# Kernel tuning notes

Measured on AMD Instinct MI355X. Metric: run time of the kernel, lower is better.

## Reference

```python
import jax, jax.numpy as jnp
import numpy as np

N = 50000      # nodes (single node type 'mapping_var')
IN = 128       # in_feats
HID = 128      # hid_feats
OUT = 64       # out_feats
R = 3          # number of relations
E = 800000     # edges per relation (avg degree 16)
NEG_SLOPE = 0.01  # F.leaky_relu default


def setup_inputs() -> dict:
    key = jax.random.key(0)
    ks = jax.random.split(key, 9)
    s = 0.05
    return {
        "x": jax.random.normal(ks[0], (N, IN), jnp.float32),
        "edge_src": jax.random.randint(ks[1], (R, E), 0, N, jnp.int32),
        "edge_dst": jax.random.randint(ks[2], (R, E), 0, N, jnp.int32),
        "W0": jax.random.normal(ks[3], (R, IN, HID), jnp.float32) * s,
        "b0": jnp.zeros((R, HID), jnp.float32),
        "Wl": jax.random.normal(ks[4], (4, R, HID, HID), jnp.float32) * s,
        "bl": jnp.zeros((4, R, HID), jnp.float32),
        "Wout": jax.random.normal(ks[5], (HID, OUT), jnp.float32) * s,
        "bout": jnp.zeros((OUT,), jnp.float32),
    }


def _hetero_conv(h, edge_src, edge_dst, W, b):
    """One HeteroGraphConv layer: per-relation GraphConv (norm='both') then
    mean-aggregate across relations.  h: [N, Din], W: [R, Din, Dout]."""
    ones = jnp.ones((E,), h.dtype)
    outs = []
    for r in range(R):
        src, dst = edge_src[r], edge_dst[r]
        out_deg = jax.ops.segment_sum(ones, src, num_segments=N)
        in_deg = jax.ops.segment_sum(ones, dst, num_segments=N)
        # src-side normalization D_out^{-1/2}
        hn = h * jax.lax.rsqrt(jnp.maximum(out_deg, 1.0))[:, None]
        # gather messages along edges, sum into destinations
        agg = jax.ops.segment_sum(hn[src], dst, num_segments=N)
        # dst-side normalization D_in^{-1/2}
        agg = agg * jax.lax.rsqrt(jnp.maximum(in_deg, 1.0))[:, None]
        outs.append(agg @ W[r] + b[r])
    return jnp.mean(jnp.stack(outs, axis=0), axis=0)  # 'mean' cross-relation aggregate


def reference(x, edge_src, edge_dst, W0, b0, Wl, bl, Wout, bout):
    # Layer 0: in_feats -> hid_feats
    h = _hetero_conv(x, edge_src, edge_dst, W0, b0)
    h = jax.nn.leaky_relu(h, NEG_SLOPE)  # dropout omitted (eval mode)
    # Layers 1..4: hid -> hid; activation after all but the last
    for l in range(4):
        h = _hetero_conv(h, edge_src, edge_dst, Wl[l], bl[l])
        if l != 3:
            h = jax.nn.leaky_relu(h, NEG_SLOPE)
    # final Linear on h['mapping_var']
    return h @ Wout + bout
```

## Files before the change

### kernel.cpp

```cpp
#include <hip/hip_runtime.h>
#include <hip/hip_bf16.h>
#include <cstddef>
#include <cstdint>

#define NNODES 50000
#define NR 3
#define NE 800000
#define HIDF 128
#define OUTF 64
#define NEG_SLOPE 0.01f
#define SCAN_T 1024
#define NCHUNK ((NNODES + SCAN_T - 1) / SCAN_T)
#define KTOT (NR * HIDF)
#define KU (KTOT / 2)
#define RN (NR * NNODES)
#define CHN 4096
#define NCH ((NNODES + CHN - 1) / CHN)
#define NSEG 8
#define SEGE (NE / NSEG)

__device__ __forceinline__ float bf_lo(uint v) { return __uint_as_float(v << 16); }
__device__ __forceinline__ float bf_hi(uint v) { return __uint_as_float(v & 0xffff0000u); }
__device__ __forceinline__ uint bf_rne(float f) {
    uint u = __float_as_uint(f);
    return (u + 0x7fffu + ((u >> 16) & 1u)) >> 16;
}
__device__ __forceinline__ uint bf_pack(float a, float b) {
    return bf_rne(a) | (bf_rne(b) << 16);
}

typedef short bf16x8 __attribute__((ext_vector_type(8)));
typedef float f32x4 __attribute__((ext_vector_type(4)));
__device__ __forceinline__ bf16x8 as_bf(uint4 v) { return __builtin_bit_cast(bf16x8, v); }

__global__ __launch_bounds__(256) void k_cast_x(const float* __restrict__ x,
                                                uint* __restrict__ xb) {
    int i = blockIdx.x * blockDim.x + threadIdx.x;
    if (i >= NNODES * (HIDF / 2)) return;
    float2 v = *(const float2*)(x + (size_t)i * 2);
    xb[i] = bf_pack(v.x, v.y);
}

__global__ __launch_bounds__(256) void k_cast_w(const float* __restrict__ W0,
                                                const float* __restrict__ Wl,
                                                uint* __restrict__ wbT) {
    int idx = blockIdx.x * blockDim.x + threadIdx.x;
    if (idx >= 5 * HIDF * KU) return;
    int l = idx / (HIDF * KU);
    int rem = idx - l * (HIDF * KU);
    int t = rem / HIDF;
    int n = rem - t * HIDF;
    int r = t / 64;
    int kk = (t - r * 64) * 2;
    const float* Wsrc = (l == 0) ? W0 : Wl + (size_t)(l - 1) * NR * HIDF * HIDF;
    const float* wp = Wsrc + ((size_t)r * HIDF + kk) * HIDF + n;
    float a = wp[0];
    float b = wp[HIDF];
    wbT[(size_t)l * HIDF * KU + (size_t)n * KU + t] = bf_pack(a, b);
}

__global__ __launch_bounds__(1024) void k_seg_count(const int* __restrict__ esrc,
                                                    const int* __restrict__ edst,
                                                    int* __restrict__ sc_out,
                                                    int* __restrict__ sc_in) {
    __shared__ int cnt[CHN];
    int bid = blockIdx.x;
    int role = bid / (NR * NCH * NSEG);
    int rem = bid - role * (NR * NCH * NSEG);
    int r = rem / (NCH * NSEG);
    int rem2 = rem - r * (NCH * NSEG);
    int c = rem2 / NSEG;
    int seg = rem2 - c * NSEG;
    int lo = c * CHN;
    int hi = lo + CHN; if (hi > NNODES) hi = NNODES;
    int span = hi - lo;
    const int* arr = (role ? esrc : edst) + (size_t)r * NE + (size_t)seg * SEGE;

    for (int i = threadIdx.x; i < CHN; i += 1024) cnt[i] = 0;
    __syncthreads();

    int base = threadIdx.x * 4;
    for (int it = 0; it < SEGE; it += 4096) {
        int idx = it + base;
        if (idx < SEGE) {
            int4 v = *(const int4*)(arr + idx);
            if ((unsigned)(v.x - lo) < (unsigned)span) atomicAdd(&cnt[v.x - lo], 1);
            if ((unsigned)(v.y - lo) < (unsigned)span) atomicAdd(&cnt[v.y - lo], 1);
            if ((unsigned)(v.z - lo) < (unsigned)span) atomicAdd(&cnt[v.z - lo], 1);
            if ((unsigned)(v.w - lo) < (unsigned)span) atomicAdd(&cnt[v.w - lo], 1);
        }
    }
    __syncthreads();

    int* dst = (role ? sc_out : sc_in) + (size_t)seg * RN + r * NNODES;
    for (int i = threadIdx.x; i < span; i += 1024) dst[lo + i] = cnt[i];
}

__global__ __launch_bounds__(256) void k_merge(const int* __restrict__ sc_out,
                                               const int* __restrict__ sc_in,
                                               int* __restrict__ deg_in,
                                               int* __restrict__ xsoff,
                                               float* __restrict__ out_norm,
                                               float* __restrict__ in_norm) {
    int idx = blockIdx.x * blockDim.x + threadIdx.x;
    if (idx >= RN) return;
    int so = 0;
#pragma unroll
    for (int s = 0; s < NSEG; ++s) so += sc_out[(size_t)s * RN + idx];
    int si = 0;
#pragma unroll
    for (int s = 0; s < NSEG; ++s) {
        xsoff[(size_t)s * RN + idx] = si;
        si += sc_in[(size_t)s * RN + idx];
    }
    deg_in[idx] = si;
    out_norm[idx] = rsqrtf((float)(so > 1 ? so : 1));
    in_norm[idx]  = rsqrtf((float)(si > 1 ? si : 1));
}

__global__ __launch_bounds__(SCAN_T) void k_scan1(const int* __restrict__ deg_in,
                                                  int* __restrict__ row_ptr,
                                                  int* __restrict__ csums) {
    __shared__ int buf[SCAN_T];
    int r = blockIdx.x / NCHUNK;
    int c = blockIdx.x % NCHUNK;
    int tid = threadIdx.x;
    int i = c * SCAN_T + tid;
    int v = (i < NNODES) ? deg_in[r * NNODES + i] : 0;
    buf[tid] = v;
    __syncthreads();
    for (int off = 1; off < SCAN_T; off <<= 1) {
        int t = (tid >= off) ? buf[tid - off] : 0;
        __syncthreads();
        buf[tid] += t;
        __syncthreads();
    }
    if (i < NNODES) row_ptr[r * (NNODES + 1) + i + 1] = buf[tid];
    if (tid == SCAN_T - 1) csums[r * NCHUNK + c] = buf[SCAN_T - 1];
}

__global__ void k_scan2(const int* __restrict__ csums, int* __restrict__ coffs) {
    int r = threadIdx.x;
    if (r >= NR) return;
    int run = 0;
    for (int c = 0; c < NCHUNK; ++c) {
        coffs[r * NCHUNK + c] = run;
        run += csums[r * NCHUNK + c];
    }
}

__global__ __launch_bounds__(SCAN_T) void k_scan3(int* __restrict__ row_ptr,
                                                  const int* __restrict__ coffs) {
    int r = blockIdx.x / NCHUNK;
    int c = blockIdx.x % NCHUNK;
    int tid = threadIdx.x;
    int i = c * SCAN_T + tid;
    int off = coffs[r * NCHUNK + c];
    if (i < NNODES) row_ptr[r * (NNODES + 1) + i + 1] += off;
    if (tid == 0 && c == 0) row_ptr[r * (NNODES + 1)] = 0;
}

__global__ __launch_bounds__(1024) void k_seg_fill(const int* __restrict__ esrc,
                                                   const int* __restrict__ edst,
                                                   const int* __restrict__ row_ptr,
                                                   const int* __restrict__ xsoff,
                                                   const float* __restrict__ out_norm,
                                                   int2* __restrict__ csr_sw) {
    __shared__ int cur[CHN];
    int bid = blockIdx.x;
    int r = bid / (NCH * NSEG);
    int rem = bid - r * (NCH * NSEG);
    int c = rem / NSEG;
    int seg = rem - c * NSEG;
    int lo = c * CHN;
    int hi = lo + CHN; if (hi > NNODES) hi = NNODES;
    int span = hi - lo;
    const int* sarr = esrc + (size_t)r * NE + (size_t)seg * SEGE;
    const int* darr = edst + (size_t)r * NE + (size_t)seg * SEGE;
    const int* rp = row_ptr + r * (NNODES + 1);
    const int* xs = xsoff + (size_t)seg * RN + r * NNODES;
    const float* on = out_norm + r * NNODES;
    int2* cs = csr_sw + (size_t)r * NE;

    for (int i = threadIdx.x; i < CHN; i += 1024) cur[i] = 0;
    __syncthreads();

    int base = threadIdx.x * 4;
    for (int it = 0; it < SEGE; it += 4096) {
        int idx = it + base;
        if (idx < SEGE) {
            int4 d = *(const int4*)(darr + idx);
            int4 s = *(const int4*)(sarr + idx);
            if ((unsigned)(d.x - lo) < (unsigned)span) {
                int p = atomicAdd(&cur[d.x - lo], 1);
                cs[rp[d.x] + xs[d.x] + p] = make_int2(s.x, __float_as_int(on[s.x]));
            }
            if ((unsigned)(d.y - lo) < (unsigned)span) {
                int p = atomicAdd(&cur[d.y - lo], 1);
                cs[rp[d.y] + xs[d.y] + p] = make_int2(s.y, __float_as_int(on[s.y]));
            }
            if ((unsigned)(d.z - lo) < (unsigned)span) {
                int p = atomicAdd(&cur[d.z - lo], 1);
                cs[rp[d.z] + xs[d.z] + p] = make_int2(s.z, __float_as_int(on[s.z]));
            }
            if ((unsigned)(d.w - lo) < (unsigned)span) {
                int p = atomicAdd(&cur[d.w - lo], 1);
                cs[rp[d.w] + xs[d.w] + p] = make_int2(s.w, __float_as_int(on[s.w]));
            }
        }
    }
}

__global__ __launch_bounds__(256) void k_aggregate(const uint* __restrict__ hin,
                                                   const float* __restrict__ in_norm,
                                                   const int* __restrict__ row_ptr,
                                                   const int2* __restrict__ csr_sw,
                                                   uint* __restrict__ aggb) {
    int wave = blockIdx.x * 4 + (threadIdx.x >> 6);
    if (wave >= RN) return;
    int r = wave / NNODES;
    int n = wave - r * NNODES;
    int lane = threadIdx.x & 63;
    int quarter = lane >> 4;
    int sub = lane & 15;
    int start = row_ptr[r * (NNODES + 1) + n];
    int end   = row_ptr[r * (NNODES + 1) + n + 1];
    const int2* cw = csr_sw + (size_t)r * NE;

    float acc[8];
#pragma unroll
    for (int k = 0; k < 8; ++k) acc[k] = 0.f;

    int i = start;
    int last = end - 1;
    for (; i + 16 <= end; i += 16) {
        int2 e0 = cw[i + quarter];
        int2 e1 = cw[i + 4 + quarter];
        int2 e2 = cw[i + 8 + quarter];
        int2 e3 = cw[i + 12 + quarter];
        uint4 v0 = *(const uint4*)(hin + (size_t)e0.x * (HIDF / 2) + sub * 4);
        uint4 v1 = *(const uint4*)(hin + (size_t)e1.x * (HIDF / 2) + sub * 4);
        uint4 v2 = *(const uint4*)(hin + (size_t)e2.x * (HIDF / 2) + sub * 4);
        uint4 v3 = *(const uint4*)(hin + (size_t)e3.x * (HIDF / 2) + sub * 4);
        float w0 = __int_as_float(e0.y);
        float w1 = __int_as_float(e1.y);
        float w2 = __int_as_float(e2.y);
        float w3 = __int_as_float(e3.y);
        acc[0] = fmaf(w0, bf_lo(v0.x), acc[0]); acc[1] = fmaf(w0, bf_hi(v0.x), acc[1]);
        acc[2] = fmaf(w0, bf_lo(v0.y), acc[2]); acc[3] = fmaf(w0, bf_hi(v0.y), acc[3]);
        acc[4] = fmaf(w0, bf_lo(v0.z), acc[4]); acc[5] = fmaf(w0, bf_hi(v0.z), acc[5]);
        acc[6] = fmaf(w0, bf_lo(v0.w), acc[6]); acc[7] = fmaf(w0, bf_hi(v0.w), acc[7]);
        acc[0] = fmaf(w1, bf_lo(v1.x), acc[0]); acc[1] = fmaf(w1, bf_hi(v1.x), acc[1]);
        acc[2] = fmaf(w1, bf_lo(v1.y), acc[2]); acc[3] = fmaf(w1, bf_hi(v1.y), acc[3]);
        acc[4] = fmaf(w1, bf_lo(v1.z), acc[4]); acc[5] = fmaf(w1, bf_hi(v1.z), acc[5]);
        acc[6] = fmaf(w1, bf_lo(v1.w), acc[6]); acc[7] = fmaf(w1, bf_hi(v1.w), acc[7]);
        acc[0] = fmaf(w2, bf_lo(v2.x), acc[0]); acc[1] = fmaf(w2, bf_hi(v2.x), acc[1]);
        acc[2] = fmaf(w2, bf_lo(v2.y), acc[2]); acc[3] = fmaf(w2, bf_hi(v2.y), acc[3]);
        acc[4] = fmaf(w2, bf_lo(v2.z), acc[4]); acc[5] = fmaf(w2, bf_hi(v2.z), acc[5]);
        acc[6] = fmaf(w2, bf_lo(v2.w), acc[6]); acc[7] = fmaf(w2, bf_hi(v2.w), acc[7]);
        acc[0] = fmaf(w3, bf_lo(v3.x), acc[0]); acc[1] = fmaf(w3, bf_hi(v3.x), acc[1]);
        acc[2] = fmaf(w3, bf_lo(v3.y), acc[2]); acc[3] = fmaf(w3, bf_hi(v3.y), acc[3]);
        acc[4] = fmaf(w3, bf_lo(v3.z), acc[4]); acc[5] = fmaf(w3, bf_hi(v3.z), acc[5]);
        acc[6] = fmaf(w3, bf_lo(v3.w), acc[6]); acc[7] = fmaf(w3, bf_hi(v3.w), acc[7]);
    }
    for (; i + 8 <= end; i += 8) {
        int2 eA = cw[i + quarter];
        int2 eB = cw[i + 4 + quarter];
        uint4 vA = *(const uint4*)(hin + (size_t)eA.x * (HIDF / 2) + sub * 4);
        uint4 vB = *(const uint4*)(hin + (size_t)eB.x * (HIDF / 2) + sub * 4);
        float wA = __int_as_float(eA.y);
        float wB = __int_as_float(eB.y);
        acc[0] = fmaf(wA, bf_lo(vA.x), acc[0]); acc[1] = fmaf(wA, bf_hi(vA.x), acc[1]);
        acc[2] = fmaf(wA, bf_lo(vA.y), acc[2]); acc[3] = fmaf(wA, bf_hi(vA.y), acc[3]);
        acc[4] = fmaf(wA, bf_lo(vA.z), acc[4]); acc[5] = fmaf(wA, bf_hi(vA.z), acc[5]);
        acc[6] = fmaf(wA, bf_lo(vA.w), acc[6]); acc[7] = fmaf(wA, bf_hi(vA.w), acc[7]);
        acc[0] = fmaf(wB, bf_lo(vB.x), acc[0]); acc[1] = fmaf(wB, bf_hi(vB.x), acc[1]);
        acc[2] = fmaf(wB, bf_lo(vB.y), acc[2]); acc[3] = fmaf(wB, bf_hi(vB.y), acc[3]);
        acc[4] = fmaf(wB, bf_lo(vB.z), acc[4]); acc[5] = fmaf(wB, bf_hi(vB.z), acc[5]);
        acc[6] = fmaf(wB, bf_lo(vB.w), acc[6]); acc[7] = fmaf(wB, bf_hi(vB.w), acc[7]);
    }
    for (; i < end; i += 4) {
        int e_idx = i + quarter;
        bool live = e_idx < end;
        int2 e = cw[live ? e_idx : last];
        float w = live ? __int_as_float(e.y) : 0.f;
        uint4 v = *(const uint4*)(hin + (size_t)e.x * (HIDF / 2) + sub * 4);
        acc[0] = fmaf(w, bf_lo(v.x), acc[0]); acc[1] = fmaf(w, bf_hi(v.x), acc[1]);
        acc[2] = fmaf(w, bf_lo(v.y), acc[2]); acc[3] = fmaf(w, bf_hi(v.y), acc[3]);
        acc[4] = fmaf(w, bf_lo(v.z), acc[4]); acc[5] = fmaf(w, bf_hi(v.z), acc[5]);
        acc[6] = fmaf(w, bf_lo(v.w), acc[6]); acc[7] = fmaf(w, bf_hi(v.w), acc[7]);
    }

#pragma unroll
    for (int k = 0; k < 8; ++k) {
        acc[k] += __shfl_xor(acc[k], 16);
        acc[k] += __shfl_xor(acc[k], 32);
    }

    if (quarter == 0) {
        float wn = in_norm[r * NNODES + n];
        uint4 pk;
        pk.x = bf_pack(acc[0] * wn, acc[1] * wn);
        pk.y = bf_pack(acc[2] * wn, acc[3] * wn);
        pk.z = bf_pack(acc[4] * wn, acc[5] * wn);
        pk.w = bf_pack(acc[6] * wn, acc[7] * wn);
        *(uint4*)(aggb + (size_t)n * KU + r * (HIDF / 2) + sub * 4) = pk;
    }
}

__global__ __launch_bounds__(256) void k_conv_mm(const uint* __restrict__ aggb,
                                                 const uint* __restrict__ wbT,
                                                 const float* __restrict__ bias,
                                                 ushort* __restrict__ hout,
                                                 int act) {
    int wv   = threadIdx.x >> 6;
    int lane = threadIdx.x & 63;
    int lrow = lane & 15;
    int kgrp = lane >> 4;
    int rb = blockIdx.x * 128 + wv * 32;

    f32x4 acc[2][8];
#pragma unroll
    for (int m = 0; m < 2; ++m)
#pragma unroll
        for (int nr = 0; nr < 8; ++nr) acc[m][nr] = (f32x4){0.f, 0.f, 0.f, 0.f};

    int row0 = rb + lrow;
    int row1 = rb + 16 + lrow;
    bool v0 = row0 < NNODES;
    bool v1 = row1 < NNODES;
    const uint* a0p = aggb + (size_t)row0 * KU + kgrp * 4;
    const uint* a1p = aggb + (size_t)row1 * KU + kgrp * 4;
    const uint* bp  = wbT + (size_t)lrow * KU + kgrp * 4;
    const uint4 za = make_uint4(0u, 0u, 0u, 0u);

#pragma unroll
    for (int ks = 0; ks < KTOT / 32; ++ks) {
        uint4 ua0 = v0 ? *(const uint4*)(a0p + ks * 16) : za;
        uint4 ua1 = v1 ? *(const uint4*)(a1p + ks * 16) : za;
        bf16x8 af0 = as_bf(ua0);
        bf16x8 af1 = as_bf(ua1);
#pragma unroll
        for (int nr = 0; nr < 8; ++nr) {
            uint4 ub = *(const uint4*)(bp + (size_t)nr * (16 * KU) + ks * 16);
            bf16x8 bf = as_bf(ub);
            acc[0][nr] = __builtin_amdgcn_mfma_f32_16x16x32_bf16(af0, bf, acc[0][nr], 0, 0, 0);
            acc[1][nr] = __builtin_amdgcn_mfma_f32_16x16x32_bf16(af1, bf, acc[1][nr], 0, 0, 0);
        }
    }

    const float inv3 = 1.f / 3.f;
#pragma unroll
    for (int nr = 0; nr < 8; ++nr) {
        int col = nr * 16 + lrow;
        float bm = (bias[col] + bias[HIDF + col] + bias[2 * HIDF + col]) * inv3;
#pragma unroll
        for (int m = 0; m < 2; ++m) {
            int rbase = rb + m * 16 + kgrp * 4;
#pragma unroll
            for (int i = 0; i < 4; ++i) {
                int row = rbase + i;
                if (row >= NNODES) continue;
                float t = acc[m][nr][i] * inv3 + bm;
                if (act) t = (t > 0.f) ? t : NEG_SLOPE * t;
                hout[(size_t)row * HIDF + col] = (ushort)bf_rne(t);
            }
        }
    }
}

__global__ __launch_bounds__(256) void k_final(const uint* __restrict__ h,
                                               const float* __restrict__ Wout,
                                               const float* __restrict__ bout,
                                               float* __restrict__ out) {
    int tid = threadIdx.x;
    int col = tid & 63;
    int row = blockIdx.x * 4 + (tid >> 6);
    if (row >= NNODES) return;
    const uint* hp = h + (size_t)row * (HIDF / 2);
    float acc = bout[col];
#pragma unroll 8
    for (int ku = 0; ku < HIDF / 2; ++ku) {
        uint v = hp[ku];
        acc = fmaf(bf_lo(v), Wout[(2 * ku) * OUTF + col], acc);
        acc = fmaf(bf_hi(v), Wout[(2 * ku + 1) * OUTF + col], acc);
    }
    out[(size_t)row * OUTF + col] = acc;
}

extern "C" void kernel_launch(void* const* d_in, const int* in_sizes, int n_in,
                              void* d_out, int out_size, void* d_ws, size_t ws_size,
                              hipStream_t stream) {
    const float* x    = (const float*)d_in[0];
    const int*   esrc = (const int*)d_in[1];
    const int*   edst = (const int*)d_in[2];
    const float* W0   = (const float*)d_in[3];
    const float* b0   = (const float*)d_in[4];
    const float* Wl   = (const float*)d_in[5];
    const float* bl   = (const float*)d_in[6];
    const float* Wout = (const float*)d_in[7];
    const float* bout = (const float*)d_in[8];
    float* out = (float*)d_out;

    char* ws = (char*)d_ws;
    size_t off = 0;
    auto carve = [&](size_t bytes) {
        size_t p = off;
        off += (bytes + 255) & ~(size_t)255;
        return p;
    };
    const size_t SZ_RN_I = (size_t)RN * 4;
    size_t o_sc_out  = carve((size_t)NSEG * RN * 4);
    size_t o_sc_in   = carve((size_t)NSEG * RN * 4);
    size_t o_xsoff   = carve((size_t)NSEG * RN * 4);
    size_t o_deg_in  = carve(SZ_RN_I);
    size_t o_out_nrm = carve(SZ_RN_I);
    size_t o_in_nrm  = carve(SZ_RN_I);
    size_t o_row_ptr = carve((size_t)NR * (NNODES + 1) * 4);
    size_t o_csums   = carve((size_t)NR * NCHUNK * 4);
    size_t o_coffs   = carve((size_t)NR * NCHUNK * 4);
    size_t o_csr     = carve((size_t)NR * NE * 8);
    size_t o_aggb    = carve((size_t)NNODES * KU * 4);
    size_t o_xb      = carve((size_t)NNODES * (HIDF / 2) * 4);
    size_t o_h       = carve((size_t)NNODES * (HIDF / 2) * 4);
    size_t o_wbT     = carve((size_t)5 * HIDF * KU * 4);
    (void)ws_size;

    int*    sc_out   = (int*)(ws + o_sc_out);
    int*    sc_in    = (int*)(ws + o_sc_in);
    int*    xsoff    = (int*)(ws + o_xsoff);
    int*    deg_in   = (int*)(ws + o_deg_in);
    float*  out_norm = (float*)(ws + o_out_nrm);
    float*  in_norm  = (float*)(ws + o_in_nrm);
    int*    row_ptr  = (int*)(ws + o_row_ptr);
    int*    csums    = (int*)(ws + o_csums);
    int*    coffs    = (int*)(ws + o_coffs);
    int2*   csr_sw   = (int2*)(ws + o_csr);
    uint*   aggb     = (uint*)(ws + o_aggb);
    uint*   xb       = (uint*)(ws + o_xb);
    uint*   h        = (uint*)(ws + o_h);
    uint*   wbT      = (uint*)(ws + o_wbT);


    k_cast_x<<<(NNODES * (HIDF / 2) + 255) / 256, 256, 0, stream>>>(x, xb);
    k_cast_w<<<(5 * HIDF * KU + 255) / 256, 256, 0, stream>>>(W0, Wl, wbT);
    k_seg_count<<<2 * NR * NCH * NSEG, 1024, 0, stream>>>(esrc, edst, sc_out, sc_in);
    k_merge<<<(RN + 255) / 256, 256, 0, stream>>>(sc_out, sc_in, deg_in, xsoff, out_norm, in_norm);
    k_scan1<<<NR * NCHUNK, SCAN_T, 0, stream>>>(deg_in, row_ptr, csums);
    k_scan2<<<1, 64, 0, stream>>>(csums, coffs);
    k_scan3<<<NR * NCHUNK, SCAN_T, 0, stream>>>(row_ptr, coffs);
    k_seg_fill<<<NR * NCH * NSEG, 1024, 0, stream>>>(esrc, edst, row_ptr, xsoff, out_norm, csr_sw);

    const int aggBlocks = (RN + 3) / 4;
    const int mmBlocks  = (NNODES + 127) / 128;

    const uint* hin = xb;
    for (int l = 0; l < 5; ++l) {
        k_aggregate<<<aggBlocks, 256, 0, stream>>>(hin, in_norm, row_ptr, csr_sw, aggb);
        const uint*  Wp = wbT + (size_t)l * HIDF * KU;
        const float* bp = (l == 0) ? b0 : bl + (size_t)(l - 1) * NR * HIDF;
        k_conv_mm<<<mmBlocks, 256, 0, stream>>>(aggb, Wp, bp, (ushort*)h, (l < 4) ? 1 : 0);
        hin = h;
    }
    k_final<<<(NNODES + 3) / 4, 256, 0, stream>>>(h, Wout, bout, out);
}
```

Measured before the change: 928.4 us.

## Split aggregate feature dimension into quarters across blocks with 16-edge parallelism

The aggregation kernel now gives each wave one quarter (32 features) of a node-relation row instead of the full row. Lanes are regrouped as 16 edges × 4 lanes, so more edges are gathered per step and each gather is a narrower 64-byte slice. Block IDs are interleaved so that the four quarter-blocks of the same nodes run close together, which is meant to raise memory-level parallelism on short degree-16 rows and improve L2 reuse. In exchange, the CSR edge list is read four times and cross-lane reduction needs two more shuffle stages.

After: 1.620 ms. 74.5% more time.

```diff
diff --git a/kernel.cpp b/kernel.cpp
--- a/kernel.cpp
+++ b/kernel.cpp
@@ -18,6 +18,7 @@
 #define NCH ((NNODES + CHN - 1) / CHN)
 #define NSEG 8
 #define SEGE (NE / NSEG)
+#define AGG_BPP 18750
 
 __device__ __forceinline__ float bf_lo(uint v) { return __uint_as_float(v << 16); }
 __device__ __forceinline__ float bf_hi(uint v) { return __uint_as_float(v & 0xffff0000u); }
@@ -216,16 +217,22 @@
                                                    const int* __restrict__ row_ptr,
                                                    const int2* __restrict__ csr_sw,
                                                    uint* __restrict__ aggb) {
-    int wave = blockIdx.x * 4 + (threadIdx.x >> 6);
-    if (wave >= RN) return;
-    int r = wave / NNODES;
-    int n = wave - r * NNODES;
+    int bid = blockIdx.x;
+    int slot = bid & 7;
+    int q = slot >> 1;
+    int j = (bid >> 3) * 2 + (slot & 1);
+    int wv = threadIdx.x >> 6;
+    int unit = j * 4 + wv;
+    if (unit >= RN) return;
+    int r = unit / NNODES;
+    int n = unit - r * NNODES;
     int lane = threadIdx.x & 63;
-    int quarter = lane >> 4;
-    int sub = lane & 15;
+    int g = lane >> 2;
+    int sub4 = lane & 3;
     int start = row_ptr[r * (NNODES + 1) + n];
     int end   = row_ptr[r * (NNODES + 1) + n + 1];
     const int2* cw = csr_sw + (size_t)r * NE;
+    int qoff = q * 16 + sub4 * 4;
 
     float acc[8];
 #pragma unroll
@@ -233,41 +240,11 @@
 
     int i = start;
     int last = end - 1;
-    for (; i + 16 <= end; i += 16) {
-        int2 e0 = cw[i + quarter];
-        int2 e1 = cw[i + 4 + quarter];
-        int2 e2 = cw[i + 8 + quarter];
-        int2 e3 = cw[i + 12 + quarter];
-        uint4 v0 = *(const uint4*)(hin + (size_t)e0.x * (HIDF / 2) + sub * 4);
-        uint4 v1 = *(const uint4*)(hin + (size_t)e1.x * (HIDF / 2) + sub * 4);
-        uint4 v2 = *(const uint4*)(hin + (size_t)e2.x * (HIDF / 2) + sub * 4);
-        uint4 v3 = *(const uint4*)(hin + (size_t)e3.x * (HIDF / 2) + sub * 4);
-        float w0 = __int_as_float(e0.y);
-        float w1 = __int_as_float(e1.y);
-        float w2 = __int_as_float(e2.y);
-        float w3 = __int_as_float(e3.y);
-        acc[0] = fmaf(w0, bf_lo(v0.x), acc[0]); acc[1] = fmaf(w0, bf_hi(v0.x), acc[1]);
-        acc[2] = fmaf(w0, bf_lo(v0.y), acc[2]); acc[3] = fmaf(w0, bf_hi(v0.y), acc[3]);
-        acc[4] = fmaf(w0, bf_lo(v0.z), acc[4]); acc[5] = fmaf(w0, bf_hi(v0.z), acc[5]);
-        acc[6] = fmaf(w0, bf_lo(v0.w), acc[6]); acc[7] = fmaf(w0, bf_hi(v0.w), acc[7]);
-        acc[0] = fmaf(w1, bf_lo(v1.x), acc[0]); acc[1] = fmaf(w1, bf_hi(v1.x), acc[1]);
-        acc[2] = fmaf(w1, bf_lo(v1.y), acc[2]); acc[3] = fmaf(w1, bf_hi(v1.y), acc[3]);
-        acc[4] = fmaf(w1, bf_lo(v1.z), acc[4]); acc[5] = fmaf(w1, bf_hi(v1.z), acc[5]);
-        acc[6] = fmaf(w1, bf_lo(v1.w), acc[6]); acc[7] = fmaf(w1, bf_hi(v1.w), acc[7]);
-        acc[0] = fmaf(w2, bf_lo(v2.x), acc[0]); acc[1] = fmaf(w2, bf_hi(v2.x), acc[1]);
-        acc[2] = fmaf(w2, bf_lo(v2.y), acc[2]); acc[3] = fmaf(w2, bf_hi(v2.y), acc[3]);
-        acc[4] = fmaf(w2, bf_lo(v2.z), acc[4]); acc[5] = fmaf(w2, bf_hi(v2.z), acc[5]);
-        acc[6] = fmaf(w2, bf_lo(v2.w), acc[6]); acc[7] = fmaf(w2, bf_hi(v2.w), acc[7]);
-        acc[0] = fmaf(w3, bf_lo(v3.x), acc[0]); acc[1] = fmaf(w3, bf_hi(v3.x), acc[1]);
-        acc[2] = fmaf(w3, bf_lo(v3.y), acc[2]); acc[3] = fmaf(w3, bf_hi(v3.y), acc[3]);
-        acc[4] = fmaf(w3, bf_lo(v3.z), acc[4]); acc[5] = fmaf(w3, bf_hi(v3.z), acc[5]);
-        acc[6] = fmaf(w3, bf_lo(v3.w), acc[6]); acc[7] = fmaf(w3, bf_hi(v3.w), acc[7]);
-    }
-    for (; i + 8 <= end; i += 8) {
-        int2 eA = cw[i + quarter];
-        int2 eB = cw[i + 4 + quarter];
-        uint4 vA = *(const uint4*)(hin + (size_t)eA.x * (HIDF / 2) + sub * 4);
-        uint4 vB = *(const uint4*)(hin + (size_t)eB.x * (HIDF / 2) + sub * 4);
+    for (; i + 32 <= end; i += 32) {
+        int2 eA = cw[i + g];
+        int2 eB = cw[i + 16 + g];
+        uint4 vA = *(const uint4*)(hin + (size_t)eA.x * (HIDF / 2) + qoff);
+        uint4 vB = *(const uint4*)(hin + (size_t)eB.x * (HIDF / 2) + qoff);
         float wA = __int_as_float(eA.y);
         float wB = __int_as_float(eB.y);
         acc[0] = fmaf(wA, bf_lo(vA.x), acc[0]); acc[1] = fmaf(wA, bf_hi(vA.x), acc[1]);
@@ -279,12 +256,12 @@
         acc[4] = fmaf(wB, bf_lo(vB.z), acc[4]); acc[5] = fmaf(wB, bf_hi(vB.z), acc[5]);
         acc[6] = fmaf(wB, bf_lo(vB.w), acc[6]); acc[7] = fmaf(wB, bf_hi(vB.w), acc[7]);
     }
-    for (; i < end; i += 4) {
-        int e_idx = i + quarter;
-        bool live = e_idx < end;
-        int2 e = cw[live ? e_idx : last];
+    for (; i < end; i += 16) {
+        int ei = i + g;
+        bool live = ei < end;
+        int2 e = cw[live ? ei : last];
         float w = live ? __int_as_float(e.y) : 0.f;
-        uint4 v = *(const uint4*)(hin + (size_t)e.x * (HIDF / 2) + sub * 4);
+        uint4 v = *(const uint4*)(hin + (size_t)e.x * (HIDF / 2) + qoff);
         acc[0] = fmaf(w, bf_lo(v.x), acc[0]); acc[1] = fmaf(w, bf_hi(v.x), acc[1]);
         acc[2] = fmaf(w, bf_lo(v.y), acc[2]); acc[3] = fmaf(w, bf_hi(v.y), acc[3]);
         acc[4] = fmaf(w, bf_lo(v.z), acc[4]); acc[5] = fmaf(w, bf_hi(v.z), acc[5]);
@@ -293,18 +270,20 @@
 
 #pragma unroll
     for (int k = 0; k < 8; ++k) {
+        acc[k] += __shfl_xor(acc[k], 4);
+        acc[k] += __shfl_xor(acc[k], 8);
         acc[k] += __shfl_xor(acc[k], 16);
         acc[k] += __shfl_xor(acc[k], 32);
     }
 
-    if (quarter == 0) {
+    if (g == 0) {
         float wn = in_norm[r * NNODES + n];
         uint4 pk;
         pk.x = bf_pack(acc[0] * wn, acc[1] * wn);
         pk.y = bf_pack(acc[2] * wn, acc[3] * wn);
         pk.z = bf_pack(acc[4] * wn, acc[5] * wn);
         pk.w = bf_pack(acc[6] * wn, acc[7] * wn);
-        *(uint4*)(aggb + (size_t)n * KU + r * (HIDF / 2) + sub * 4) = pk;
+        *(uint4*)(aggb + (size_t)n * KU + r * (HIDF / 2) + qoff) = pk;
     }
 }
 
@@ -451,7 +430,7 @@
     k_scan3<<<NR * NCHUNK, SCAN_T, 0, stream>>>(row_ptr, coffs);
     k_seg_fill<<<NR * NCH * NSEG, 1024, 0, stream>>>(esrc, edst, row_ptr, xsoff, out_norm, csr_sw);
 
-    const int aggBlocks = (RN + 3) / 4;
+    const int aggBlocks = AGG_BPP * 8;
     const int mmBlocks  = (NNODES + 127) / 128;
 
     const uint* hin = xb;
```
